# Kernel optimization log

Measured on AMD Instinct MI355X. Metric: run time of the kernel, lower is better.

Reference implementation:

```python
import jax, jax.numpy as jnp
import numpy as np

B, S, D, F, R = 128, 128, 512, 84, 32
DS = D // 8      # priori (projected) dim = 64
NE = 3           # number of RefExperts actually constructed
H = D // 64      # 8 heads for both nn.MultiheadAttention modules and feat SDPA
NEG = -1e9


def ln(x, g, b, eps=1e-5):
    m = x.mean(-1, keepdims=True)
    v = ((x - m) ** 2).mean(-1, keepdims=True)
    return (x - m) * jax.lax.rsqrt(v + eps) * g + b


def mha(q, k, v, Wi, bi, Wo, bo, h, mask=None):
    # torch nn.MultiheadAttention with packed in_proj (stored here as [D,3D])
    Dm = q.shape[-1]
    dh = Dm // h
    qp = (q @ Wi[:, :Dm] + bi[:Dm]).reshape(q.shape[0], q.shape[1], h, dh)
    kp = (k @ Wi[:, Dm:2 * Dm] + bi[Dm:2 * Dm]).reshape(k.shape[0], k.shape[1], h, dh)
    vp = (v @ Wi[:, 2 * Dm:] + bi[2 * Dm:]).reshape(v.shape[0], v.shape[1], h, dh)
    s = jnp.einsum('bqhd,bkhd->bhqk', qp, kp) / np.float32(np.sqrt(dh))
    if mask is not None:
        s = jnp.where(mask, NEG, s)
    o = jnp.einsum('bhqk,bkhd->bqhd', jax.nn.softmax(s, -1), vp)
    return o.reshape(q.shape[0], q.shape[1], Dm) @ Wo + bo


def forward(hidden_states, tag_hidden_state, feats, refs,
            W_moe, b_moe, Wg, bg, Wq_e, Wk_e, Wv_e, Wo_e,
            g_np, b_np, Wi_p, bi_p, Wo_p, bo_p, W_pe, b_pe,
            g_nh, b_nh, Wi_f, bi_f, Wo_f, bo_f,
            g_nfh, b_nfh, Wq_a, bq_a, Wk_a, bk_a, Wv_a, bv_a, Wd, bd, g_ln, b_ln):
    seq = tag_hidden_state.shape[1]
    causal = jnp.triu(jnp.ones((seq, seq), bool), 1)  # torch triu(diag=1).bool()
    # ---- MOE priori: project tags, soft-gate 3 reference cross-attn experts ----
    xs = tag_hidden_state @ W_moe + b_moe                 # [B,S,DS]
    gate = jax.nn.softmax(xs @ Wg + bg, -1)               # [B,S,NE]
    q = jnp.einsum('bsd,edk->ebsk', xs, Wq_e)             # [E,B,S,DS]
    k = jnp.einsum('ebrf,efk->ebrk', refs, Wk_e)          # [E,B,R,DS]
    v = jnp.einsum('ebrf,efk->ebrk', refs, Wv_e)
    s = jnp.einsum('ebsk,ebrk->ebsr', q, k) / np.float32(np.sqrt(DS))
    eo = jnp.einsum('ebsr,ebrk->ebsk', jax.nn.softmax(s, -1), v)
    eo = jnp.einsum('ebsk,ekm->ebsm', eo, Wo_e)           # [E,B,S,DS]
    priori = jnp.einsum('ebsd,bse->bsd', eo, gate)        # [B,S,DS]
    # ---- priori causal self-attention (pre-LN residual) ----
    npri = ln(priori, g_np, b_np)
    priori = mha(npri, npri, npri, Wi_p, bi_p, Wo_p, bo_p, H, causal) + priori
    priori = priori @ W_pe + b_pe                         # [B,S,D]
    # ---- fusion cross-attention: hidden attends to priori (causal) ----
    npri = ln(priori, g_nh, b_nh)
    hidden_states = mha(hidden_states, npri, npri, Wi_f, bi_f, Wo_f, bo_f, H, causal) + hidden_states
    # ---- feat cross-attention block (MultiHeadAttention wrapper, post-LN) ----
    nh = ln(hidden_states, g_nfh, b_nfh)
    dh = D // H
    qp = (nh @ Wq_a + bq_a).reshape(B, seq, H, dh)
    kp = (feats @ Wk_a + bk_a).reshape(B, F, H, dh)
    vp = (feats @ Wv_a + bv_a).reshape(B, F, H, dh)
    s2 = jnp.einsum('bqhd,bkhd->bhqk', qp, kp) / np.float32(np.sqrt(dh))
    ctx = jnp.einsum('bhqk,bkhd->bqhd', jax.nn.softmax(s2, -1), vp).reshape(B, seq, D)
    ctx = ctx @ Wd + bd                                   # dense; dropout is eval-mode identity
    return ln(ctx + nh, g_ln, b_ln, 1e-12)                # skip connection + post-LN (eps=1e-12)


def setup_inputs() -> dict:
    key = jax.random.key(0)
    ks = jax.random.split(key, 40)
    p = lambda i, shp: (jax.random.normal(ks[i], shp, jnp.float32) * 0.02)
    inp = {
        'hidden_states': jax.random.normal(ks[0], (B, S, D), jnp.float32),
        'tag_hidden_state': jax.random.normal(ks[1], (B, S, D), jnp.float32),
        'feats': jax.random.normal(ks[2], (B, F, D), jnp.float32),
        'refs': jax.random.normal(ks[3], (NE, B, R, D), jnp.float32),
        'W_moe': p(4, (D, DS)), 'b_moe': jnp.zeros((DS,)),
        'Wg': p(5, (DS, NE)), 'bg': jnp.zeros((NE,)),
        'Wq_e': p(6, (NE, DS, DS)), 'Wk_e': p(7, (NE, D, DS)),
        'Wv_e': p(8, (NE, D, DS)), 'Wo_e': p(9, (NE, DS, DS)),
        'g_np': jnp.ones((DS,)), 'b_np': jnp.zeros((DS,)),
        'Wi_p': p(10, (DS, 3 * DS)), 'bi_p': jnp.zeros((3 * DS,)),
        'Wo_p': p(11, (DS, DS)), 'bo_p': jnp.zeros((DS,)),
        'W_pe': p(12, (DS, D)), 'b_pe': jnp.zeros((D,)),
        'g_nh': jnp.ones((D,)), 'b_nh': jnp.zeros((D,)),
        'Wi_f': p(13, (D, 3 * D)), 'bi_f': jnp.zeros((3 * D,)),
        'Wo_f': p(14, (D, D)), 'bo_f': jnp.zeros((D,)),
        'g_nfh': jnp.ones((D,)), 'b_nfh': jnp.zeros((D,)),
        'Wq_a': p(15, (D, D)), 'bq_a': jnp.zeros((D,)),
        'Wk_a': p(16, (D, D)), 'bk_a': jnp.zeros((D,)),
        'Wv_a': p(17, (D, D)), 'bv_a': jnp.zeros((D,)),
        'Wd': p(18, (D, D)), 'bd': jnp.zeros((D,)),
        'g_ln': jnp.ones((D,)), 'b_ln': jnp.zeros((D,)),
    }
    return inp


def reference(hidden_states, tag_hidden_state, feats, refs,
              W_moe, b_moe, Wg, bg, Wq_e, Wk_e, Wv_e, Wo_e,
              g_np, b_np, Wi_p, bi_p, Wo_p, bo_p, W_pe, b_pe,
              g_nh, b_nh, Wi_f, bi_f, Wo_f, bo_f,
              g_nfh, b_nfh, Wq_a, bq_a, Wk_a, bk_a, Wv_a, bv_a, Wd, bd, g_ln, b_ln):
    return forward(hidden_states, tag_hidden_state, feats, refs,
                   W_moe, b_moe, Wg, bg, Wq_e, Wk_e, Wv_e, Wo_e,
                   g_np, b_np, Wi_p, bi_p, Wo_p, bo_p, W_pe, b_pe,
                   g_nh, b_nh, Wi_f, bi_f, Wo_f, bo_f,
                   g_nfh, b_nfh, Wq_a, bq_a, Wk_a, bk_a, Wv_a, bv_a, Wd, bd, g_ln, b_ln)
```

## Files before the change

kernel.cpp:

```cpp
#include <hip/hip_runtime.h>
#include <hip/hip_bf16.h>

typedef unsigned short u16;
typedef unsigned int   u32;
typedef __attribute__((ext_vector_type(8))) short short8;
typedef __attribute__((ext_vector_type(4))) float f32x4;

#define BBt 128
#define SS 128
#define RR 32
#define NEx 3
#define MB (1024 * 1024)

static __device__ __forceinline__ float bs2f(u16 u){ return __uint_as_float(((u32)u) << 16); }
static __device__ __forceinline__ float blo(u32 u){ return __uint_as_float(u << 16); }
static __device__ __forceinline__ float bhi(u32 u){ return __uint_as_float(u & 0xffff0000u); }
static __device__ __forceinline__ u16 f2bs(float x){
    u32 u = __float_as_uint(x);
    u += 0x7fff + ((u >> 16) & 1);
    return (u16)(u >> 16);
}
static __device__ __forceinline__ float ldany(const float* p){ return *p; }
static __device__ __forceinline__ float ldany(const u16* p){ return bs2f(*p); }

template<typename TA, typename TRes, typename TC>
__global__ __launch_bounds__(256) void gemm_mfma(
    const TA* __restrict__ A, int lda, long long sA,
    const float* __restrict__ W, int ldw, long long sW,
    const float* __restrict__ bias,
    const TRes* __restrict__ Res, int ldr,
    TC* __restrict__ C, int ldc, long long sC,
    int K, int Ncols)
{
    int bz = blockIdx.z;
    A += (long long)bz * sA;
    W += (long long)bz * sW;
    C += (long long)bz * sC;

    __shared__ __align__(16) u16 As[128][40];
    __shared__ __align__(16) u16 Bs[128][40];

    int tid = threadIdx.x;
    long long row0 = (long long)blockIdx.y * 128;
    int col0 = blockIdx.x * 128;

    int wid = tid >> 6, lane = tid & 63;
    int wm = (wid >> 1) * 64, wn = (wid & 1) * 64;
    int l15 = lane & 15, quad = lane >> 4;

    f32x4 acc[4][4];
    #pragma unroll
    for (int i = 0; i < 4; ++i)
        #pragma unroll
        for (int j = 0; j < 4; ++j)
            acc[i][j] = (f32x4){0.f, 0.f, 0.f, 0.f};

    int ar = tid >> 1, ak = (tid & 1) * 16;
    int bk0 = (tid & 15) * 2, bn0 = (tid >> 4) * 8;

    for (int kt = 0; kt < K; kt += 32) {
        {
            const TA* src = A + (row0 + ar) * lda + kt + ak;
            if constexpr (sizeof(TA) == 4) {
                u16 tmp[16];
                #pragma unroll
                for (int t = 0; t < 16; t += 4) {
                    float4 f = *(const float4*)(src + t);
                    tmp[t] = f2bs(f.x); tmp[t+1] = f2bs(f.y);
                    tmp[t+2] = f2bs(f.z); tmp[t+3] = f2bs(f.w);
                }
                *(uint4*)&As[ar][ak]     = *(const uint4*)&tmp[0];
                *(uint4*)&As[ar][ak + 8] = *(const uint4*)&tmp[8];
            } else {
                *(uint4*)&As[ar][ak]     = *(const uint4*)(src);
                *(uint4*)&As[ar][ak + 8] = *(const uint4*)(src + 8);
            }
        }
        {
            if (col0 + bn0 < Ncols) {
                const float* w0 = W + (long long)(kt + bk0) * ldw + col0 + bn0;
                const float* w1 = w0 + ldw;
                float r0[8], r1[8];
                *(float4*)&r0[0] = *(const float4*)(w0);
                *(float4*)&r0[4] = *(const float4*)(w0 + 4);
                *(float4*)&r1[0] = *(const float4*)(w1);
                *(float4*)&r1[4] = *(const float4*)(w1 + 4);
                #pragma unroll
                for (int i = 0; i < 8; ++i) {
                    u32 packed = (u32)f2bs(r0[i]) | ((u32)f2bs(r1[i]) << 16);
                    *(u32*)&Bs[bn0 + i][bk0] = packed;
                }
            } else {
                #pragma unroll
                for (int i = 0; i < 8; ++i)
                    *(u32*)&Bs[bn0 + i][bk0] = 0u;
            }
        }
        __syncthreads();

        short8 af[4], bfr[4];
        #pragma unroll
        for (int mt = 0; mt < 4; ++mt)
            af[mt] = *(const short8*)&As[wm + mt * 16 + l15][quad * 8];
        #pragma unroll
        for (int nt = 0; nt < 4; ++nt)
            bfr[nt] = *(const short8*)&Bs[wn + nt * 16 + l15][quad * 8];
        #pragma unroll
        for (int mt = 0; mt < 4; ++mt)
            #pragma unroll
            for (int nt = 0; nt < 4; ++nt)
                acc[mt][nt] = __builtin_amdgcn_mfma_f32_16x16x32_bf16(
                    af[mt], bfr[nt], acc[mt][nt], 0, 0, 0);
        __syncthreads();
    }

    #pragma unroll
    for (int mt = 0; mt < 4; ++mt) {
        #pragma unroll
        for (int r = 0; r < 4; ++r) {
            long long row = row0 + wm + mt * 16 + quad * 4 + r;
            #pragma unroll
            for (int nt = 0; nt < 4; ++nt) {
                int col = col0 + wn + nt * 16 + l15;
                if (col >= Ncols) continue;
                float v = acc[mt][nt][r];
                if (bias) v += bias[col];
                if (Res)  v += ldany(&Res[row * ldr + col]);
                if constexpr (sizeof(TC) == 4) C[row * ldc + col] = v;
                else                           C[row * ldc + col] = f2bs(v);
            }
        }
    }
}

__global__ __launch_bounds__(256) void attn_mfma_k(
    const u16* __restrict__ Q, const u16* __restrict__ K,
    const u16* __restrict__ V, u16* __restrict__ out,
    int L, int causal)
{
    int h = blockIdx.x, b = blockIdx.y;
    int tid = threadIdx.x;
    int w = tid >> 6, lane = tid & 63;
    int l15 = lane & 15, quad = lane >> 4;

    int NTP = (L + 15) >> 4;
    int Lp  = NTP * 16;
    int ntmax = causal ? (2 * w + 1) : (NTP - 1);
    int ksmax = causal ? w : (((L + 31) >> 5) - 1);

    __shared__ __align__(16) u16 vT[64][136];
    __shared__ __align__(16) u16 pool[4][32][136];
    u16 (*kS)[72] = (u16(*)[72])&pool[0][0][0];

    for (int i = tid; i < Lp * 8; i += 256) {
        int r = i >> 3, c8 = i & 7;
        uint4 val = {0u, 0u, 0u, 0u};
        if (r < L) val = *(const uint4*)&K[((long long)b * L + r) * 512 + h * 64 + c8 * 8];
        *(uint4*)&kS[r][c8 * 8] = val;
    }
    for (int i = tid; i < 512; i += 256) {
        int kp = i & 63, dg = i >> 6;
        int kv0 = kp * 2;
        if (kv0 < Lp) {
            uint4 r0 = {0u,0u,0u,0u}, r1 = {0u,0u,0u,0u};
            if (kv0 < L)     r0 = *(const uint4*)&V[((long long)b * L + kv0    ) * 512 + h * 64 + dg * 8];
            if (kv0 + 1 < L) r1 = *(const uint4*)&V[((long long)b * L + kv0 + 1) * 512 + h * 64 + dg * 8];
            u32 w0[4] = {r0.x, r0.y, r0.z, r0.w};
            u32 w1[4] = {r1.x, r1.y, r1.z, r1.w};
            #pragma unroll
            for (int j = 0; j < 4; ++j) {
                *(u32*)&vT[dg * 8 + 2 * j    ][kv0] = (w0[j] & 0xffffu) | (w1[j] << 16);
                *(u32*)&vT[dg * 8 + 2 * j + 1][kv0] = (w0[j] >> 16) | (w1[j] & 0xffff0000u);
            }
        }
    }

    short8 qf[2][2];
    #pragma unroll
    for (int mt = 0; mt < 2; ++mt)
        #pragma unroll
        for (int ks = 0; ks < 2; ++ks)
            qf[mt][ks] = *(const short8*)&Q[((long long)b * 128 + w * 32 + mt * 16 + l15) * 512
                                            + h * 64 + ks * 32 + quad * 8];
    __syncthreads();

    f32x4 sacc[2][8];
    #pragma unroll
    for (int mt = 0; mt < 2; ++mt)
        #pragma unroll
        for (int nt = 0; nt < 8; ++nt)
            sacc[mt][nt] = (f32x4){0.f, 0.f, 0.f, 0.f};
    #pragma unroll
    for (int nt = 0; nt < 8; ++nt) {
        if (nt <= ntmax) {
            short8 kf0 = *(const short8*)&kS[nt * 16 + l15][quad * 8];
            short8 kf1 = *(const short8*)&kS[nt * 16 + l15][32 + quad * 8];
            #pragma unroll
            for (int mt = 0; mt < 2; ++mt) {
                sacc[mt][nt] = __builtin_amdgcn_mfma_f32_16x16x32_bf16(qf[mt][0], kf0, sacc[mt][nt], 0, 0, 0);
                sacc[mt][nt] = __builtin_amdgcn_mfma_f32_16x16x32_bf16(qf[mt][1], kf1, sacc[mt][nt], 0, 0, 0);
            }
        }
    }

    float pm[2][4], ls[2][4];
    #pragma unroll
    for (int mt = 0; mt < 2; ++mt) {
        #pragma unroll
        for (int r = 0; r < 4; ++r) pm[mt][r] = -1e30f;
        #pragma unroll
        for (int nt = 0; nt < 8; ++nt) {
            if (nt <= ntmax) {
                int col = nt * 16 + l15;
                #pragma unroll
                for (int r = 0; r < 4; ++r) {
                    int rowq = w * 32 + mt * 16 + quad * 4 + r;
                    bool bad = (col >= L) || (causal && col > rowq);
                    float sv = bad ? -1e30f : sacc[mt][nt][r];
                    sacc[mt][nt][r] = sv;
                    pm[mt][r] = fmaxf(pm[mt][r], sv);
                }
            }
        }
        #pragma unroll
        for (int r = 0; r < 4; ++r) {
            float mx = pm[mt][r];
            #pragma unroll
            for (int o = 1; o <= 8; o <<= 1) mx = fmaxf(mx, __shfl_xor(mx, o));
            pm[mt][r] = mx * 0.125f;
            ls[mt][r] = 0.f;
        }
        #pragma unroll
        for (int nt = 0; nt < 8; ++nt) {
            if (nt <= ntmax) {
                #pragma unroll
                for (int r = 0; r < 4; ++r) {
                    float p = __expf(fmaf(sacc[mt][nt][r], 0.125f, -pm[mt][r]));
                    sacc[mt][nt][r] = p;
                    ls[mt][r] += p;
                }
            }
        }
        #pragma unroll
        for (int r = 0; r < 4; ++r) {
            float sm = ls[mt][r];
            #pragma unroll
            for (int o = 1; o <= 8; o <<= 1) sm += __shfl_xor(sm, o);
            ls[mt][r] = 1.f / sm;
        }
    }

    __syncthreads();

    u16 (*pW)[136] = (u16(*)[136])&pool[w][0][0];
    bool wl = (l15 & 1) == 0;
    #pragma unroll
    for (int mt = 0; mt < 2; ++mt)
        #pragma unroll
        for (int nt = 0; nt < 8; ++nt) {
            if (nt <= ntmax) {
                #pragma unroll
                for (int r = 0; r < 4; ++r) {
                    float pv = sacc[mt][nt][r];
                    float po = __shfl_xor(pv, 1);
                    if (wl) {
                        u32 packed = (u32)f2bs(pv) | ((u32)f2bs(po) << 16);
                        *(u32*)&pW[mt * 16 + quad * 4 + r][nt * 16 + l15] = packed;
                    }
                }
            }
        }

    f32x4 oacc[2][4];
    #pragma unroll
    for (int mt = 0; mt < 2; ++mt)
        #pragma unroll
        for (int nd = 0; nd < 4; ++nd)
            oacc[mt][nd] = (f32x4){0.f, 0.f, 0.f, 0.f};
    #pragma unroll
    for (int ks = 0; ks < 4; ++ks) {
        if (ks <= ksmax) {
            short8 pf0 = *(const short8*)&pW[l15     ][ks * 32 + quad * 8];
            short8 pf1 = *(const short8*)&pW[16 + l15][ks * 32 + quad * 8];
            #pragma unroll
            for (int nd = 0; nd < 4; ++nd) {
                short8 vf = *(const short8*)&vT[nd * 16 + l15][ks * 32 + quad * 8];
                oacc[0][nd] = __builtin_amdgcn_mfma_f32_16x16x32_bf16(pf0, vf, oacc[0][nd], 0, 0, 0);
                oacc[1][nd] = __builtin_amdgcn_mfma_f32_16x16x32_bf16(pf1, vf, oacc[1][nd], 0, 0, 0);
            }
        }
    }

    #pragma unroll
    for (int mt = 0; mt < 2; ++mt)
        #pragma unroll
        for (int nd = 0; nd < 4; ++nd)
            #pragma unroll
            for (int r = 0; r < 4; ++r) {
                float ov = oacc[mt][nd][r] * ls[mt][r];
                float oo = __shfl_xor(ov, 1);
                if (wl) {
                    long long rowq = (long long)b * 128 + w * 32 + mt * 16 + quad * 4 + r;
                    u32 packed = (u32)f2bs(ov) | ((u32)f2bs(oo) << 16);
                    *(u32*)&out[rowq * 512 + h * 64 + nd * 16 + l15] = packed;
                }
            }
}

template<typename TI, typename TO>
__global__ __launch_bounds__(256) void ln512_t(
    const TI* __restrict__ x, const float* __restrict__ g,
    const float* __restrict__ bt, TO* __restrict__ y, float eps)
{
    int row = blockIdx.x, tid = threadIdx.x;
    long long base = (long long)row * 512;
    float v0 = ldany(&x[base + tid]);
    float v1 = ldany(&x[base + 256 + tid]);
    float s = v0 + v1, ss = v0 * v0 + v1 * v1;
    #pragma unroll
    for (int o = 32; o >= 1; o >>= 1) { s += __shfl_xor(s, o); ss += __shfl_xor(ss, o); }
    __shared__ float red[2][4];
    int wave = tid >> 6, lane = tid & 63;
    if (lane == 0) { red[0][wave] = s; red[1][wave] = ss; }
    __syncthreads();
    s  = red[0][0] + red[0][1] + red[0][2] + red[0][3];
    ss = red[1][0] + red[1][1] + red[1][2] + red[1][3];
    float mean = s * (1.f / 512.f);
    float var = ss * (1.f / 512.f) - mean * mean;
    float rstd = rsqrtf(fmaxf(var, 0.f) + eps);
    float o0 = (v0 - mean) * rstd * g[tid]       + bt[tid];
    float o1 = (v1 - mean) * rstd * g[256 + tid] + bt[256 + tid];
    if constexpr (sizeof(TO) == 4) { y[base + tid] = o0; y[base + 256 + tid] = o1; }
    else { y[base + tid] = f2bs(o0); y[base + 256 + tid] = f2bs(o1); }
}

__global__ __launch_bounds__(128) void moe_attn_k(
    const float* __restrict__ qe,
    const float* __restrict__ ke,
    const float* __restrict__ ve,
    const float* __restrict__ xs,
    const float* __restrict__ Wg,
    const float* __restrict__ bg,
    float* __restrict__ geo)
{
    int e = blockIdx.x, b = blockIdx.y;
    int tid = threadIdx.x;
    __shared__ __align__(16) float kS[RR][64];
    __shared__ __align__(16) float vS[RR][64];

    {
        const float4* ks = (const float4*)&ke[((long long)e * (BBt * RR) + (long long)b * RR) * 64];
        const float4* vs = (const float4*)&ve[((long long)e * (BBt * RR) + (long long)b * RR) * 64];
        float4* kd = (float4*)&kS[0][0];
        float4* vd = (float4*)&vS[0][0];
        #pragma unroll
        for (int t = 0; t < 4; ++t) {
            kd[tid + 128 * t] = ks[tid + 128 * t];
            vd[tid + 128 * t] = vs[tid + 128 * t];
        }
    }

    long long row = (long long)b * SS + tid;
    float q[64];
    {
        const float4* qp = (const float4*)&qe[((long long)e * (BBt * SS) + row) * 64];
        #pragma unroll
        for (int t = 0; t < 16; ++t) {
            float4 f = qp[t];
            q[4*t] = f.x; q[4*t+1] = f.y; q[4*t+2] = f.z; q[4*t+3] = f.w;
        }
    }

    float l0 = bg[0], l1 = bg[1], l2 = bg[2];
    {
        const float4* xr = (const float4*)&xs[row * 64];
        #pragma unroll
        for (int t = 0; t < 16; ++t) {
            float4 f = xr[t];
            float xv[4] = {f.x, f.y, f.z, f.w};
            #pragma unroll
            for (int u = 0; u < 4; ++u) {
                int j = 4 * t + u;
                l0 = fmaf(xv[u], Wg[j * 3 + 0], l0);
                l1 = fmaf(xv[u], Wg[j * 3 + 1], l1);
                l2 = fmaf(xv[u], Wg[j * 3 + 2], l2);
            }
        }
    }
    float mg = fmaxf(l0, fmaxf(l1, l2));
    float g0 = __expf(l0 - mg), g1 = __expf(l1 - mg), g2 = __expf(l2 - mg);
    float gate = (e == 0 ? g0 : (e == 1 ? g1 : g2)) / (g0 + g1 + g2);

    __syncthreads();

    float s[RR];
    #pragma unroll
    for (int r = 0; r < RR; ++r) {
        float a0 = 0.f, a1 = 0.f, a2 = 0.f, a3 = 0.f;
        const float4* kr = (const float4*)&kS[r][0];
        #pragma unroll
        for (int t = 0; t < 16; ++t) {
            float4 f = kr[t];
            a0 = fmaf(q[4*t],   f.x, a0);
            a1 = fmaf(q[4*t+1], f.y, a1);
            a2 = fmaf(q[4*t+2], f.z, a2);
            a3 = fmaf(q[4*t+3], f.w, a3);
        }
        s[r] = ((a0 + a1) + (a2 + a3)) * 0.125f;
    }
    float m = s[0];
    #pragma unroll
    for (int r = 1; r < RR; ++r) m = fmaxf(m, s[r]);
    float l = 0.f;
    #pragma unroll
    for (int r = 0; r < RR; ++r) { s[r] = __expf(s[r] - m); l += s[r]; }
    float scale = gate / l;

    float acc[64];
    #pragma unroll
    for (int d = 0; d < 64; ++d) acc[d] = 0.f;
    #pragma unroll
    for (int r = 0; r < RR; ++r) {
        float p = s[r];
        const float4* vr = (const float4*)&vS[r][0];
        #pragma unroll
        for (int t = 0; t < 16; ++t) {
            float4 f = vr[t];
            acc[4*t]   = fmaf(p, f.x, acc[4*t]);
            acc[4*t+1] = fmaf(p, f.y, acc[4*t+1]);
            acc[4*t+2] = fmaf(p, f.z, acc[4*t+2]);
            acc[4*t+3] = fmaf(p, f.w, acc[4*t+3]);
        }
    }
    float4* op = (float4*)&geo[row * 192 + e * 64];
    #pragma unroll
    for (int t = 0; t < 16; ++t) {
        float4 f;
        f.x = acc[4*t] * scale;   f.y = acc[4*t+1] * scale;
        f.z = acc[4*t+2] * scale; f.w = acc[4*t+3] * scale;
        op[t] = f;
    }
}

__global__ __launch_bounds__(128) void attn_small_k(
    const float* __restrict__ qkv, float* __restrict__ out)
{
    int h = blockIdx.x, b = blockIdx.y;
    int tid = threadIdx.x;
    __shared__ float kS[SS][9], vS[SS][9];
    long long base = ((long long)b * SS + tid) * 192;
    #pragma unroll
    for (int d = 0; d < 8; ++d) {
        kS[tid][d] = qkv[base + 64 + h * 8 + d];
        vS[tid][d] = qkv[base + 128 + h * 8 + d];
    }
    float q[8];
    #pragma unroll
    for (int d = 0; d < 8; ++d)
        q[d] = qkv[base + h * 8 + d] * 0.35355339059327373f;
    __syncthreads();

    float m = -1e30f, l = 0.f, acc[8] = {};
    for (int j = 0; j <= tid; ++j) {
        float s = 0.f;
        #pragma unroll
        for (int d = 0; d < 8; ++d) s = fmaf(q[d], kS[j][d], s);
        float mn = fmaxf(m, s);
        float corr = __expf(m - mn);
        float p = __expf(s - mn);
        l = l * corr + p;
        #pragma unroll
        for (int d = 0; d < 8; ++d) acc[d] = fmaf(p, vS[j][d], acc[d] * corr);
        m = mn;
    }
    float inv = 1.f / l;
    #pragma unroll
    for (int d = 0; d < 8; ++d)
        out[((long long)b * SS + tid) * 64 + h * 8 + d] = acc[d] * inv;
}

__global__ __launch_bounds__(256) void ln64_k(
    const float* __restrict__ x, const float* __restrict__ g,
    const float* __restrict__ bt, float* __restrict__ y, int M)
{
    int wave = threadIdx.x >> 6, lane = threadIdx.x & 63;
    int row = blockIdx.x * 4 + wave;
    if (row >= M) return;
    long long base = (long long)row * 64;
    float v = x[base + lane];
    float s = v, ss = v * v;
    #pragma unroll
    for (int o = 32; o >= 1; o >>= 1) { s += __shfl_xor(s, o); ss += __shfl_xor(ss, o); }
    float mean = s * (1.f / 64.f);
    float var = ss * (1.f / 64.f) - mean * mean;
    float rstd = rsqrtf(fmaxf(var, 0.f) + 1e-5f);
    y[base + lane] = (v - mean) * rstd * g[lane] + bt[lane];
}

extern "C" void kernel_launch(void* const* d_in, const int* in_sizes, int n_in,
                              void* d_out, int out_size, void* d_ws, size_t ws_size,
                              hipStream_t stream)
{
    (void)in_sizes; (void)n_in; (void)out_size; (void)ws_size;
    const float* hidden = (const float*)d_in[0];
    const float* tag    = (const float*)d_in[1];
    const float* feats  = (const float*)d_in[2];
    const float* refs   = (const float*)d_in[3];
    const float* W_moe  = (const float*)d_in[4];
    const float* b_moe  = (const float*)d_in[5];
    const float* Wg     = (const float*)d_in[6];
    const float* bg     = (const float*)d_in[7];
    const float* Wq_e   = (const float*)d_in[8];
    const float* Wk_e   = (const float*)d_in[9];
    const float* Wv_e   = (const float*)d_in[10];
    const float* Wo_e   = (const float*)d_in[11];
    const float* g_np   = (const float*)d_in[12];
    const float* b_np   = (const float*)d_in[13];
    const float* Wi_p   = (const float*)d_in[14];
    const float* bi_p   = (const float*)d_in[15];
    const float* Wo_p   = (const float*)d_in[16];
    const float* bo_p   = (const float*)d_in[17];
    const float* W_pe   = (const float*)d_in[18];
    const float* b_pe   = (const float*)d_in[19];
    const float* g_nh   = (const float*)d_in[20];
    const float* b_nh   = (const float*)d_in[21];
    const float* Wi_f   = (const float*)d_in[22];
    const float* bi_f   = (const float*)d_in[23];
    const float* Wo_f   = (const float*)d_in[24];
    const float* bo_f   = (const float*)d_in[25];
    const float* g_nfh  = (const float*)d_in[26];
    const float* b_nfh  = (const float*)d_in[27];
    const float* Wq_a   = (const float*)d_in[28];
    const float* bq_a   = (const float*)d_in[29];
    const float* Wk_a   = (const float*)d_in[30];
    const float* bk_a   = (const float*)d_in[31];
    const float* Wv_a   = (const float*)d_in[32];
    const float* bv_a   = (const float*)d_in[33];
    const float* Wd     = (const float*)d_in[34];
    const float* bd     = (const float*)d_in[35];
    const float* g_ln   = (const float*)d_in[36];
    const float* b_ln   = (const float*)d_in[37];
    float* out = (float*)d_out;
    char* ob = (char*)d_out;
    char* wb = (char*)d_ws;

    u16* W0 = (u16*)(wb + 0LL * 16 * MB);
    u16* W1 = (u16*)(wb + 1LL * 16 * MB);
    u16* O0 = (u16*)(ob + 0LL * 16 * MB);
    u16* O1 = (u16*)(ob + 1LL * 16 * MB);

    float* o_xs   = (float*)(ob + 0LL  * MB);
    float* o_ke   = (float*)(ob + 4LL  * MB);
    float* o_ve   = (float*)(ob + 7LL  * MB);
    float* o_pri  = (float*)(ob + 10LL * MB);
    float* o_np64 = (float*)(ob + 14LL * MB);
    float* o_qkv  = (float*)(ob + 18LL * MB);
    float* o_attp = (float*)(ob + 0LL  * MB);
    float* o_tmp  = (float*)(ob + 4LL  * MB);
    float* o_qe   = (float*)(wb + 0LL  * MB);
    float* o_geo  = (float*)(wb + 16LL * MB);

    dim3 blk(256);
    const float* fnull = nullptr;

    gemm_mfma<float, float, float><<<dim3(1, 128), blk, 0, stream>>>(
        tag, 512, 0, W_moe, 64, 0, b_moe, fnull, 0, o_xs, 64, 0, 512, 64);
    gemm_mfma<float, float, float><<<dim3(1, 32, 3), blk, 0, stream>>>(
        refs, 512, 4096LL * 512, Wk_e, 64, 512LL * 64, nullptr, fnull, 0,
        o_ke, 64, 4096LL * 64, 512, 64);
    gemm_mfma<float, float, float><<<dim3(1, 32, 3), blk, 0, stream>>>(
        refs, 512, 4096LL * 512, Wv_e, 64, 512LL * 64, nullptr, fnull, 0,
        o_ve, 64, 4096LL * 64, 512, 64);
    gemm_mfma<float, float, float><<<dim3(1, 128, 3), blk, 0, stream>>>(
        o_xs, 64, 0, Wq_e, 64, 4096LL, nullptr, fnull, 0,
        o_qe, 64, 16384LL * 64, 64, 64);
    moe_attn_k<<<dim3(3, 128), dim3(128), 0, stream>>>(
        o_qe, o_ke, o_ve, o_xs, Wg, bg, o_geo);
    gemm_mfma<float, float, float><<<dim3(1, 128), blk, 0, stream>>>(
        o_geo, 192, 0, Wo_e, 64, 0, nullptr, fnull, 0, o_pri, 64, 0, 192, 64);

    ln64_k<<<dim3(4096), blk, 0, stream>>>(o_pri, g_np, b_np, o_np64, 16384);
    gemm_mfma<float, float, float><<<dim3(2, 128), blk, 0, stream>>>(
        o_np64, 64, 0, Wi_p, 192, 0, bi_p, fnull, 0, o_qkv, 192, 0, 64, 192);
    attn_small_k<<<dim3(8, 128), dim3(128), 0, stream>>>(o_qkv, o_attp);
    gemm_mfma<float, float, float><<<dim3(1, 128), blk, 0, stream>>>(
        o_attp, 64, 0, Wo_p, 64, 0, bo_p, o_pri, 64, o_tmp, 64, 0, 64, 64);
    gemm_mfma<float, float, u16><<<dim3(4, 128), blk, 0, stream>>>(
        o_tmp, 64, 0, W_pe, 512, 0, b_pe, fnull, 0, W0, 512, 0, 64, 512);

    ln512_t<u16, u16><<<dim3(16384), blk, 0, stream>>>(W0, g_nh, b_nh, W0, 1e-5f);
    gemm_mfma<u16, float, u16><<<dim3(4, 128), blk, 0, stream>>>(
        W0, 512, 0, Wi_f + 512, 1536, 0, bi_f + 512, fnull, 0, O1, 512, 0, 512, 512);
    gemm_mfma<u16, float, u16><<<dim3(4, 128), blk, 0, stream>>>(
        W0, 512, 0, Wi_f + 1024, 1536, 0, bi_f + 1024, fnull, 0, W1, 512, 0, 512, 512);
    gemm_mfma<float, float, u16><<<dim3(4, 128), blk, 0, stream>>>(
        hidden, 512, 0, Wi_f, 1536, 0, bi_f, fnull, 0, O0, 512, 0, 512, 512);
    attn_mfma_k<<<dim3(8, 128), dim3(256), 0, stream>>>(O0, O1, W1, W0, 128, 1);
    gemm_mfma<u16, float, u16><<<dim3(4, 128), blk, 0, stream>>>(
        W0, 512, 0, Wo_f, 512, 0, bo_f, hidden, 512, O0, 512, 0, 512, 512);

    ln512_t<u16, u16><<<dim3(16384), blk, 0, stream>>>(O0, g_nfh, b_nfh, O0, 1e-5f);
    gemm_mfma<u16, float, u16><<<dim3(4, 128), blk, 0, stream>>>(
        O0, 512, 0, Wq_a, 512, 0, bq_a, fnull, 0, O1, 512, 0, 512, 512);
    gemm_mfma<float, float, u16><<<dim3(4, 84), blk, 0, stream>>>(
        feats, 512, 0, Wk_a, 512, 0, bk_a, fnull, 0, W0, 512, 0, 512, 512);
    gemm_mfma<float, float, u16><<<dim3(4, 84), blk, 0, stream>>>(
        feats, 512, 0, Wv_a, 512, 0, bv_a, fnull, 0, W1, 512, 0, 512, 512);
    attn_mfma_k<<<dim3(8, 128), dim3(256), 0, stream>>>(O1, W0, W1, O1, 84, 0);
    gemm_mfma<u16, u16, u16><<<dim3(4, 128), blk, 0, stream>>>(
        O1, 512, 0, Wd, 512, 0, bd, O0, 512, W0, 512, 0, 512, 512);

    ln512_t<u16, float><<<dim3(16384), blk, 0, stream>>>(W0, g_ln, b_ln, out, 1e-12f);
}
```

Measured before the change: 936.7 us.

## Stream GEMM weights directly into MFMA fragments, double-buffer A, and merge sibling projections

The GEMM kernel no longer stages the fp32 weight tile through shared memory. Each wave loads its B fragments straight from global memory and packs them with the hardware v_cvt_pk_bf16 instruction. The A tile is double-buffered in LDS, with the next tile prefetched into registers during the MFMAs, so there is one barrier per k-step. Projections that share an input (K/V of the MoE refs, K/V of the Wi_f self-attn, and K/V of feats) now run as one wider launch with split outputs, cutting launches and repeated reads of the same A. In exchange, each lane issues many strided scalar weight loads, and waves sharing a column block read the same weights twice.

New measurement: 1.369 ms. 1.46x slower.

```diff
diff --git a/kernel.cpp b/kernel.cpp
--- a/kernel.cpp
+++ b/kernel.cpp
@@ -13,32 +13,34 @@
 #define MB (1024 * 1024)
 
 static __device__ __forceinline__ float bs2f(u16 u){ return __uint_as_float(((u32)u) << 16); }
-static __device__ __forceinline__ float blo(u32 u){ return __uint_as_float(u << 16); }
-static __device__ __forceinline__ float bhi(u32 u){ return __uint_as_float(u & 0xffff0000u); }
 static __device__ __forceinline__ u16 f2bs(float x){
     u32 u = __float_as_uint(x);
     u += 0x7fff + ((u >> 16) & 1);
     return (u16)(u >> 16);
 }
+static __device__ __forceinline__ u32 pkbf(float a, float b){
+    u32 r; asm("v_cvt_pk_bf16_f32 %0, %1, %2" : "=v"(r) : "v"(a), "v"(b)); return r;
+}
 static __device__ __forceinline__ float ldany(const float* p){ return *p; }
 static __device__ __forceinline__ float ldany(const u16* p){ return bs2f(*p); }
 
 template<typename TA, typename TRes, typename TC>
-__global__ __launch_bounds__(256) void gemm_mfma(
+__global__ __launch_bounds__(256) void gemm_bb(
     const TA* __restrict__ A, int lda, long long sA,
-    const float* __restrict__ W, int ldw, long long sW,
-    const float* __restrict__ bias,
+    const float* __restrict__ W, const float* __restrict__ W2, int ldw, long long sW,
+    const float* __restrict__ bias, const float* __restrict__ bias2,
     const TRes* __restrict__ Res, int ldr,
-    TC* __restrict__ C, int ldc, long long sC,
-    int K, int Ncols)
+    TC* __restrict__ C, TC* __restrict__ C2, int ldc, long long sC,
+    int K, int Ncols, int Nsplit)
 {
     int bz = blockIdx.z;
     A += (long long)bz * sA;
     W += (long long)bz * sW;
+    if (W2) W2 += (long long)bz * sW;
     C += (long long)bz * sC;
-
-    __shared__ __align__(16) u16 As[128][40];
-    __shared__ __align__(16) u16 Bs[128][40];
+    if (C2) C2 += (long long)bz * sC;
+
+    __shared__ __align__(16) u16 As[2][128][40];
 
     int tid = threadIdx.x;
     long long row0 = (long long)blockIdx.y * 128;
@@ -56,61 +58,76 @@
             acc[i][j] = (f32x4){0.f, 0.f, 0.f, 0.f};
 
     int ar = tid >> 1, ak = (tid & 1) * 16;
-    int bk0 = (tid & 15) * 2, bn0 = (tid >> 4) * 8;
-
-    for (int kt = 0; kt < K; kt += 32) {
-        {
-            const TA* src = A + (row0 + ar) * lda + kt + ak;
+
+    {
+        const TA* src = A + (row0 + ar) * lda + ak;
+        if constexpr (sizeof(TA) == 4) {
+            float4 f0 = *(const float4*)(src);
+            float4 f1 = *(const float4*)(src + 4);
+            float4 f2 = *(const float4*)(src + 8);
+            float4 f3 = *(const float4*)(src + 12);
+            u32 t0[4] = {pkbf(f0.x,f0.y), pkbf(f0.z,f0.w), pkbf(f1.x,f1.y), pkbf(f1.z,f1.w)};
+            u32 t1[4] = {pkbf(f2.x,f2.y), pkbf(f2.z,f2.w), pkbf(f3.x,f3.y), pkbf(f3.z,f3.w)};
+            *(uint4*)&As[0][ar][ak]     = *(uint4*)t0;
+            *(uint4*)&As[0][ar][ak + 8] = *(uint4*)t1;
+        } else {
+            *(uint4*)&As[0][ar][ak]     = *(const uint4*)(src);
+            *(uint4*)&As[0][ar][ak + 8] = *(const uint4*)(src + 8);
+        }
+    }
+    __syncthreads();
+
+    int nsteps = K >> 5;
+    for (int s = 0; s < nsteps; ++s) {
+        int p = s & 1;
+        uint4 st0, st1;
+        bool have = (s + 1 < nsteps);
+        if (have) {
+            const TA* src = A + (row0 + ar) * lda + ((s + 1) << 5) + ak;
             if constexpr (sizeof(TA) == 4) {
-                u16 tmp[16];
-                #pragma unroll
-                for (int t = 0; t < 16; t += 4) {
-                    float4 f = *(const float4*)(src + t);
-                    tmp[t] = f2bs(f.x); tmp[t+1] = f2bs(f.y);
-                    tmp[t+2] = f2bs(f.z); tmp[t+3] = f2bs(f.w);
+                float4 f0 = *(const float4*)(src);
+                float4 f1 = *(const float4*)(src + 4);
+                float4 f2 = *(const float4*)(src + 8);
+                float4 f3 = *(const float4*)(src + 12);
+                u32 t0[4] = {pkbf(f0.x,f0.y), pkbf(f0.z,f0.w), pkbf(f1.x,f1.y), pkbf(f1.z,f1.w)};
+                u32 t1[4] = {pkbf(f2.x,f2.y), pkbf(f2.z,f2.w), pkbf(f3.x,f3.y), pkbf(f3.z,f3.w)};
+                st0 = *(uint4*)t0; st1 = *(uint4*)t1;
+            } else {
+                st0 = *(const uint4*)(src);
+                st1 = *(const uint4*)(src + 8);
+            }
+        }
+        short8 af[4];
+        #pragma unroll
+        for (int mt = 0; mt < 4; ++mt)
+            af[mt] = *(const short8*)&As[p][wm + mt * 16 + l15][quad * 8];
+        int kb = (s << 5) + quad * 8;
+        #pragma unroll
+        for (int nt = 0; nt < 4; ++nt) {
+            int col = col0 + wn + nt * 16 + l15;
+            const float* wp = W; int wc = col;
+            if (W2 && col >= Nsplit) { wp = W2; wc = col - Nsplit; }
+            bool ok = (col < Ncols);
+            const float* pw = wp + (long long)kb * ldw + wc;
+            union { u32 u[4]; short8 s8; } bb;
+            #pragma unroll
+            for (int i = 0; i < 4; ++i) {
+                float w0 = 0.f, w1 = 0.f;
+                if (ok) {
+                    w0 = pw[(2 * i) * ldw];
+                    w1 = pw[(2 * i + 1) * ldw];
                 }
-                *(uint4*)&As[ar][ak]     = *(const uint4*)&tmp[0];
-                *(uint4*)&As[ar][ak + 8] = *(const uint4*)&tmp[8];
-            } else {
-                *(uint4*)&As[ar][ak]     = *(const uint4*)(src);
-                *(uint4*)&As[ar][ak + 8] = *(const uint4*)(src + 8);
-            }
-        }
-        {
-            if (col0 + bn0 < Ncols) {
-                const float* w0 = W + (long long)(kt + bk0) * ldw + col0 + bn0;
-                const float* w1 = w0 + ldw;
-                float r0[8], r1[8];
-                *(float4*)&r0[0] = *(const float4*)(w0);
-                *(float4*)&r0[4] = *(const float4*)(w0 + 4);
-                *(float4*)&r1[0] = *(const float4*)(w1);
-                *(float4*)&r1[4] = *(const float4*)(w1 + 4);
-                #pragma unroll
-                for (int i = 0; i < 8; ++i) {
-                    u32 packed = (u32)f2bs(r0[i]) | ((u32)f2bs(r1[i]) << 16);
-                    *(u32*)&Bs[bn0 + i][bk0] = packed;
-                }
-            } else {
-                #pragma unroll
-                for (int i = 0; i < 8; ++i)
-                    *(u32*)&Bs[bn0 + i][bk0] = 0u;
-            }
-        }
-        __syncthreads();
-
-        short8 af[4], bfr[4];
-        #pragma unroll
-        for (int mt = 0; mt < 4; ++mt)
-            af[mt] = *(const short8*)&As[wm + mt * 16 + l15][quad * 8];
-        #pragma unroll
-        for (int nt = 0; nt < 4; ++nt)
-            bfr[nt] = *(const short8*)&Bs[wn + nt * 16 + l15][quad * 8];
-        #pragma unroll
-        for (int mt = 0; mt < 4; ++mt)
-            #pragma unroll
-            for (int nt = 0; nt < 4; ++nt)
+                bb.u[i] = pkbf(w0, w1);
+            }
+            #pragma unroll
+            for (int mt = 0; mt < 4; ++mt)
                 acc[mt][nt] = __builtin_amdgcn_mfma_f32_16x16x32_bf16(
-                    af[mt], bfr[nt], acc[mt][nt], 0, 0, 0);
+                    af[mt], bb.s8, acc[mt][nt], 0, 0, 0);
+        }
+        if (have) {
+            *(uint4*)&As[p ^ 1][ar][ak]     = st0;
+            *(uint4*)&As[p ^ 1][ar][ak + 8] = st1;
+        }
         __syncthreads();
     }
 
@@ -124,10 +141,13 @@
                 int col = col0 + wn + nt * 16 + l15;
                 if (col >= Ncols) continue;
                 float v = acc[mt][nt][r];
-                if (bias) v += bias[col];
-                if (Res)  v += ldany(&Res[row * ldr + col]);
-                if constexpr (sizeof(TC) == 4) C[row * ldc + col] = v;
-                else                           C[row * ldc + col] = f2bs(v);
+                if (bias2 && col >= Nsplit) v += bias2[col - Nsplit];
+                else if (bias)              v += bias[col];
+                if (Res) v += ldany(&Res[row * ldr + col]);
+                TC* dst = (C2 && col >= Nsplit) ? (C2 + row * ldc + (col - Nsplit))
+                                                : (C  + row * ldc + col);
+                if constexpr (sizeof(TC) == 4) *dst = v;
+                else                           *dst = f2bs(v);
             }
         }
     }
@@ -562,53 +582,59 @@
 
     dim3 blk(256);
     const float* fnull = nullptr;
-
-    gemm_mfma<float, float, float><<<dim3(1, 128), blk, 0, stream>>>(
-        tag, 512, 0, W_moe, 64, 0, b_moe, fnull, 0, o_xs, 64, 0, 512, 64);
-    gemm_mfma<float, float, float><<<dim3(1, 32, 3), blk, 0, stream>>>(
-        refs, 512, 4096LL * 512, Wk_e, 64, 512LL * 64, nullptr, fnull, 0,
-        o_ke, 64, 4096LL * 64, 512, 64);
-    gemm_mfma<float, float, float><<<dim3(1, 32, 3), blk, 0, stream>>>(
-        refs, 512, 4096LL * 512, Wv_e, 64, 512LL * 64, nullptr, fnull, 0,
-        o_ve, 64, 4096LL * 64, 512, 64);
-    gemm_mfma<float, float, float><<<dim3(1, 128, 3), blk, 0, stream>>>(
-        o_xs, 64, 0, Wq_e, 64, 4096LL, nullptr, fnull, 0,
-        o_qe, 64, 16384LL * 64, 64, 64);
+    float* f32null = nullptr;
+    u16* u16null = nullptr;
+
+    gemm_bb<float, float, float><<<dim3(1, 128), blk, 0, stream>>>(
+        tag, 512, 0, W_moe, fnull, 64, 0, b_moe, fnull, fnull, 0,
+        o_xs, f32null, 64, 0, 512, 64, 0);
+    gemm_bb<float, float, float><<<dim3(1, 32, 3), blk, 0, stream>>>(
+        refs, 512, 4096LL * 512, Wk_e, Wv_e, 64, 512LL * 64, fnull, fnull, fnull, 0,
+        o_ke, o_ve, 64, 4096LL * 64, 512, 128, 64);
+    gemm_bb<float, float, float><<<dim3(1, 128, 3), blk, 0, stream>>>(
+        o_xs, 64, 0, Wq_e, fnull, 64, 4096LL, fnull, fnull, fnull, 0,
+        o_qe, f32null, 64, 16384LL * 64, 64, 64, 0);
     moe_attn_k<<<dim3(3, 128), dim3(128), 0, stream>>>(
         o_qe, o_ke, o_ve, o_xs, Wg, bg, o_geo);
-    gemm_mfma<float, float, float><<<dim3(1, 128), blk, 0, stream>>>(
-        o_geo, 192, 0, Wo_e, 64, 0, nullptr, fnull, 0, o_pri, 64, 0, 192, 64);
+    gemm_bb<float, float, float><<<dim3(1, 128), blk, 0, stream>>>(
+        o_geo, 192, 0, Wo_e, fnull, 64, 0, fnull, fnull, fnull, 0,
+        o_pri, f32null, 64, 0, 192, 64, 0);
 
     ln64_k<<<dim3(4096), blk, 0, stream>>>(o_pri, g_np, b_np, o_np64, 16384);
-    gemm_mfma<float, float, float><<<dim3(2, 128), blk, 0, stream>>>(
-        o_np64, 64, 0, Wi_p, 192, 0, bi_p, fnull, 0, o_qkv, 192, 0, 64, 192);
+    gemm_bb<float, float, float><<<dim3(2, 128), blk, 0, stream>>>(
+        o_np64, 64, 0, Wi_p, fnull, 192, 0, bi_p, fnull, fnull, 0,
+        o_qkv, f32null, 192, 0, 64, 192, 0);
     attn_small_k<<<dim3(8, 128), dim3(128), 0, stream>>>(o_qkv, o_attp);
-    gemm_mfma<float, float, float><<<dim3(1, 128), blk, 0, stream>>>(
-        o_attp, 64, 0, Wo_p, 64, 0, bo_p, o_pri, 64, o_tmp, 64, 0, 64, 64);
-    gemm_mfma<float, float, u16><<<dim3(4, 128), blk, 0, stream>>>(
-        o_tmp, 64, 0, W_pe, 512, 0, b_pe, fnull, 0, W0, 512, 0, 64, 512);
+    gemm_bb<float, float, float><<<dim3(1, 128), blk, 0, stream>>>(
+        o_attp, 64, 0, Wo_p, fnull, 64, 0, bo_p, fnull, o_pri, 64,
+        o_tmp, f32null, 64, 0, 64, 64, 0);
+    gemm_bb<float, float, u16><<<dim3(4, 128), blk, 0, stream>>>(
+        o_tmp, 64, 0, W_pe, fnull, 512, 0, b_pe, fnull, fnull, 0,
+        W0, u16null, 512, 0, 64, 512, 0);
 
     ln512_t<u16, u16><<<dim3(16384), blk, 0, stream>>>(W0, g_nh, b_nh, W0, 1e-5f);
-    gemm_mfma<u16, float, u16><<<dim3(4, 128), blk, 0, stream>>>(
-        W0, 512, 0, Wi_f + 512, 1536, 0, bi_f + 512, fnull, 0, O1, 512, 0, 512, 512);
-    gemm_mfma<u16, float, u16><<<dim3(4, 128), blk, 0, stream>>>(
-        W0, 512, 0, Wi_f + 1024, 1536, 0, bi_f + 1024, fnull, 0, W1, 512, 0, 512, 512);
-    gemm_mfma<float, float, u16><<<dim3(4, 128), blk, 0, stream>>>(
-        hidden, 512, 0, Wi_f, 1536, 0, bi_f, fnull, 0, O0, 512, 0, 512, 512);
+    gemm_bb<u16, float, u16><<<dim3(8, 128), blk, 0, stream>>>(
+        W0, 512, 0, Wi_f + 512, fnull, 1536, 0, bi_f + 512, fnull, fnull, 0,
+        O1, W1, 512, 0, 512, 1024, 512);
+    gemm_bb<float, float, u16><<<dim3(4, 128), blk, 0, stream>>>(
+        hidden, 512, 0, Wi_f, fnull, 1536, 0, bi_f, fnull, fnull, 0,
+        O0, u16null, 512, 0, 512, 512, 0);
     attn_mfma_k<<<dim3(8, 128), dim3(256), 0, stream>>>(O0, O1, W1, W0, 128, 1);
-    gemm_mfma<u16, float, u16><<<dim3(4, 128), blk, 0, stream>>>(
-        W0, 512, 0, Wo_f, 512, 0, bo_f, hidden, 512, O0, 512, 0, 512, 512);
+    gemm_bb<u16, float, u16><<<dim3(4, 128), blk, 0, stream>>>(
+        W0, 512, 0, Wo_f, fnull, 512, 0, bo_f, fnull, hidden, 512,
+        O0, u16null, 512, 0, 512, 512, 0);
 
     ln512_t<u16, u16><<<dim3(16384), blk, 0, stream>>>(O0, g_nfh, b_nfh, O0, 1e-5f);
-    gemm_mfma<u16, float, u16><<<dim3(4, 128), blk, 0, stream>>>(
-        O0, 512, 0, Wq_a, 512, 0, bq_a, fnull, 0, O1, 512, 0, 512, 512);
-    gemm_mfma<float, float, u16><<<dim3(4, 84), blk, 0, stream>>>(
-        feats, 512, 0, Wk_a, 512, 0, bk_a, fnull, 0, W0, 512, 0, 512, 512);
-    gemm_mfma<float, float, u16><<<dim3(4, 84), blk, 0, stream>>>(
-        feats, 512, 0, Wv_a, 512, 0, bv_a, fnull, 0, W1, 512, 0, 512, 512);
+    gemm_bb<u16, float, u16><<<dim3(4, 128), blk, 0, stream>>>(
+        O0, 512, 0, Wq_a, fnull, 512, 0, bq_a, fnull, fnull, 0,
+        O1, u16null, 512, 0, 512, 512, 0);
+    gemm_bb<float, float, u16><<<dim3(8, 84), blk, 0, stream>>>(
+        feats, 512, 0, Wk_a, Wv_a, 512, 0, bk_a, bv_a, fnull, 0,
+        W0, W1, 512, 0, 512, 1024, 512);
     attn_mfma_k<<<dim3(8, 128), dim3(256), 0, stream>>>(O1, W0, W1, O1, 84, 0);
-    gemm_mfma<u16, u16, u16><<<dim3(4, 128), blk, 0, stream>>>(
-        O1, 512, 0, Wd, 512, 0, bd, O0, 512, W0, 512, 0, 512, 512);
+    gemm_bb<u16, u16, u16><<<dim3(4, 128), blk, 0, stream>>>(
+        O1, 512, 0, Wd, fnull, 512, 0, bd, fnull, O0, 512,
+        W0, u16null, 512, 0, 512, 512, 0);
 
     ln512_t<u16, float><<<dim3(16384), blk, 0, stream>>>(W0, g_ln, b_ln, out, 1e-12f);
 }
```

## Pre-transpose weights to bf16 and use vectorized GEMM loads with fused K/V projection

Applied to the files above, without the earlier changes.

Adds a small transpose-and-convert kernel that writes each weight matrix as bf16 in N-major layout. A new GEMM variant can then load B tiles with 16-byte vector reads, and it converts fp32 A with packed bf16 conversion instructions. The expert K and V projections are merged into one launch that splits its output columns into two buffers. The cost is extra transpose launches on every call, plus workspace buffers reused across stages, which adds aliasing risk.

Result: faster. 887.5 us (-5.3%).

```diff
diff --git a/kernel.cpp b/kernel.cpp
--- a/kernel.cpp
+++ b/kernel.cpp
@@ -13,15 +13,37 @@
 #define MB (1024 * 1024)
 
 static __device__ __forceinline__ float bs2f(u16 u){ return __uint_as_float(((u32)u) << 16); }
-static __device__ __forceinline__ float blo(u32 u){ return __uint_as_float(u << 16); }
-static __device__ __forceinline__ float bhi(u32 u){ return __uint_as_float(u & 0xffff0000u); }
 static __device__ __forceinline__ u16 f2bs(float x){
     u32 u = __float_as_uint(x);
     u += 0x7fff + ((u >> 16) & 1);
     return (u16)(u >> 16);
 }
+static __device__ __forceinline__ u32 pkbf(float a, float b){
+    u32 r; asm("v_cvt_pk_bf16_f32 %0, %1, %2" : "=v"(r) : "v"(a), "v"(b)); return r;
+}
 static __device__ __forceinline__ float ldany(const float* p){ return *p; }
 static __device__ __forceinline__ float ldany(const u16* p){ return bs2f(*p); }
+
+__global__ __launch_bounds__(256) void tr_bf(
+    const float* __restrict__ src, int lds_, long long sSrc,
+    u16* __restrict__ dst, long long sDst, int ldd)
+{
+    int z = blockIdx.z;
+    src += (long long)z * sSrc;
+    dst += (long long)z * sDst;
+    int n0 = blockIdx.x * 32, k0 = blockIdx.y * 32;
+    __shared__ u16 t[32][33];
+    int c = threadIdx.x & 31, r0 = threadIdx.x >> 5;
+    #pragma unroll
+    for (int i = 0; i < 4; ++i) {
+        int r = r0 + i * 8;
+        t[r][c] = f2bs(src[(long long)(k0 + r) * lds_ + n0 + c]);
+    }
+    __syncthreads();
+    int rr = threadIdx.x >> 3, kk = (threadIdx.x & 7) * 4;
+    u16 o[4] = { t[kk][rr], t[kk+1][rr], t[kk+2][rr], t[kk+3][rr] };
+    *(uint2*)&dst[(long long)(n0 + rr) * ldd + k0 + kk] = *(uint2*)o;
+}
 
 template<typename TA, typename TRes, typename TC>
 __global__ __launch_bounds__(256) void gemm_mfma(
@@ -128,6 +150,110 @@
                 if (Res)  v += ldany(&Res[row * ldr + col]);
                 if constexpr (sizeof(TC) == 4) C[row * ldc + col] = v;
                 else                           C[row * ldc + col] = f2bs(v);
+            }
+        }
+    }
+}
+
+template<typename TA, typename TRes, typename TC>
+__global__ __launch_bounds__(256) void gemm_v5(
+    const TA* __restrict__ A, int lda, long long sA,
+    const u16* __restrict__ WT, long long sW,
+    const float* __restrict__ bias, const float* __restrict__ bias2,
+    const TRes* __restrict__ Res, int ldr,
+    TC* __restrict__ C, TC* __restrict__ C2, int ldc, long long sC,
+    int K, int Ncols, int Nsplit)
+{
+    int bz = blockIdx.z;
+    A += (long long)bz * sA;
+    WT += (long long)bz * sW;
+    C += (long long)bz * sC;
+    if (C2) C2 += (long long)bz * sC;
+
+    __shared__ __align__(16) u16 As[128][40];
+    __shared__ __align__(16) u16 Bs[128][40];
+
+    int tid = threadIdx.x;
+    long long row0 = (long long)blockIdx.y * 128;
+    int col0 = blockIdx.x * 128;
+
+    int wid = tid >> 6, lane = tid & 63;
+    int wm = (wid >> 1) * 64, wn = (wid & 1) * 64;
+    int l15 = lane & 15, quad = lane >> 4;
+
+    f32x4 acc[4][4];
+    #pragma unroll
+    for (int i = 0; i < 4; ++i)
+        #pragma unroll
+        for (int j = 0; j < 4; ++j)
+            acc[i][j] = (f32x4){0.f, 0.f, 0.f, 0.f};
+
+    int ar = tid >> 1, ak = (tid & 1) * 16;
+
+    for (int kt = 0; kt < K; kt += 32) {
+        {
+            const TA* src = A + (row0 + ar) * lda + kt + ak;
+            if constexpr (sizeof(TA) == 4) {
+                float4 f0 = *(const float4*)(src);
+                float4 f1 = *(const float4*)(src + 4);
+                float4 f2 = *(const float4*)(src + 8);
+                float4 f3 = *(const float4*)(src + 12);
+                u32 t[8] = {pkbf(f0.x,f0.y), pkbf(f0.z,f0.w), pkbf(f1.x,f1.y), pkbf(f1.z,f1.w),
+                            pkbf(f2.x,f2.y), pkbf(f2.z,f2.w), pkbf(f3.x,f3.y), pkbf(f3.z,f3.w)};
+                *(uint4*)&As[ar][ak]     = *(uint4*)&t[0];
+                *(uint4*)&As[ar][ak + 8] = *(uint4*)&t[4];
+            } else {
+                *(uint4*)&As[ar][ak]     = *(const uint4*)(src);
+                *(uint4*)&As[ar][ak + 8] = *(const uint4*)(src + 8);
+            }
+        }
+        {
+            int nr = col0 + ar;
+            if (nr < Ncols) {
+                const u16* ws = WT + (long long)nr * K + kt + ak;
+                *(uint4*)&Bs[ar][ak]     = *(const uint4*)(ws);
+                *(uint4*)&Bs[ar][ak + 8] = *(const uint4*)(ws + 8);
+            } else {
+                uint4 z = {0u, 0u, 0u, 0u};
+                *(uint4*)&Bs[ar][ak] = z;
+                *(uint4*)&Bs[ar][ak + 8] = z;
+            }
+        }
+        __syncthreads();
+
+        short8 af[4], bfr[4];
+        #pragma unroll
+        for (int mt = 0; mt < 4; ++mt)
+            af[mt] = *(const short8*)&As[wm + mt * 16 + l15][quad * 8];
+        #pragma unroll
+        for (int nt = 0; nt < 4; ++nt)
+            bfr[nt] = *(const short8*)&Bs[wn + nt * 16 + l15][quad * 8];
+        #pragma unroll
+        for (int mt = 0; mt < 4; ++mt)
+            #pragma unroll
+            for (int nt = 0; nt < 4; ++nt)
+                acc[mt][nt] = __builtin_amdgcn_mfma_f32_16x16x32_bf16(
+                    af[mt], bfr[nt], acc[mt][nt], 0, 0, 0);
+        __syncthreads();
+    }
+
+    #pragma unroll
+    for (int mt = 0; mt < 4; ++mt) {
+        #pragma unroll
+        for (int r = 0; r < 4; ++r) {
+            long long row = row0 + wm + mt * 16 + quad * 4 + r;
+            #pragma unroll
+            for (int nt = 0; nt < 4; ++nt) {
+                int col = col0 + wn + nt * 16 + l15;
+                if (col >= Ncols) continue;
+                float v = acc[mt][nt][r];
+                if (bias2 && col >= Nsplit) v += bias2[col - Nsplit];
+                else if (bias)              v += bias[col];
+                if (Res) v += ldany(&Res[row * ldr + col]);
+                TC* dst = (C2 && col >= Nsplit) ? (C2 + row * ldc + (col - Nsplit))
+                                                : (C  + row * ldc + col);
+                if constexpr (sizeof(TC) == 4) *dst = v;
+                else                           *dst = f2bs(v);
             }
         }
     }
@@ -560,17 +686,29 @@
     float* o_qe   = (float*)(wb + 0LL  * MB);
     float* o_geo  = (float*)(wb + 16LL * MB);
 
+    u16* WT_moe = (u16*)(wb + 30LL * MB);
+    u16* WT_kve = (u16*)(wb + 30LL * MB + 131072);
+    u16* WT_ikv = (u16*)(ob + 0LL  * MB);
+    u16* WT_iq  = (u16*)(wb + 0LL  * MB);
+    u16* WT_of  = (u16*)(ob + 16LL * MB);
+    u16* WT_qa  = (u16*)(wb + 16LL * MB);
+    u16* WT_d   = (u16*)(wb + 16LL * MB);
+
     dim3 blk(256);
     const float* fnull = nullptr;
-
-    gemm_mfma<float, float, float><<<dim3(1, 128), blk, 0, stream>>>(
-        tag, 512, 0, W_moe, 64, 0, b_moe, fnull, 0, o_xs, 64, 0, 512, 64);
-    gemm_mfma<float, float, float><<<dim3(1, 32, 3), blk, 0, stream>>>(
-        refs, 512, 4096LL * 512, Wk_e, 64, 512LL * 64, nullptr, fnull, 0,
-        o_ke, 64, 4096LL * 64, 512, 64);
-    gemm_mfma<float, float, float><<<dim3(1, 32, 3), blk, 0, stream>>>(
-        refs, 512, 4096LL * 512, Wv_e, 64, 512LL * 64, nullptr, fnull, 0,
-        o_ve, 64, 4096LL * 64, 512, 64);
+    float* f32null = nullptr;
+    u16* u16null = nullptr;
+
+    tr_bf<<<dim3(2, 16), blk, 0, stream>>>(W_moe, 64, 0, WT_moe, 0, 512);
+    tr_bf<<<dim3(2, 16, 3), blk, 0, stream>>>(Wk_e, 64, 512LL * 64, WT_kve, 128LL * 512, 512);
+    tr_bf<<<dim3(2, 16, 3), blk, 0, stream>>>(Wv_e, 64, 512LL * 64, WT_kve + 64 * 512, 128LL * 512, 512);
+
+    gemm_v5<float, float, float><<<dim3(1, 128), blk, 0, stream>>>(
+        tag, 512, 0, WT_moe, 0, b_moe, fnull, fnull, 0,
+        o_xs, f32null, 64, 0, 512, 64, 0);
+    gemm_v5<float, float, float><<<dim3(1, 32, 3), blk, 0, stream>>>(
+        refs, 512, 4096LL * 512, WT_kve, 128LL * 512, fnull, fnull, fnull, 0,
+        o_ke, o_ve, 64, 4096LL * 64, 512, 128, 64);
     gemm_mfma<float, float, float><<<dim3(1, 128, 3), blk, 0, stream>>>(
         o_xs, 64, 0, Wq_e, 64, 4096LL, nullptr, fnull, 0,
         o_qe, 64, 16384LL * 64, 64, 64);
@@ -589,26 +727,37 @@
         o_tmp, 64, 0, W_pe, 512, 0, b_pe, fnull, 0, W0, 512, 0, 64, 512);
 
     ln512_t<u16, u16><<<dim3(16384), blk, 0, stream>>>(W0, g_nh, b_nh, W0, 1e-5f);
-    gemm_mfma<u16, float, u16><<<dim3(4, 128), blk, 0, stream>>>(
-        W0, 512, 0, Wi_f + 512, 1536, 0, bi_f + 512, fnull, 0, O1, 512, 0, 512, 512);
-    gemm_mfma<u16, float, u16><<<dim3(4, 128), blk, 0, stream>>>(
-        W0, 512, 0, Wi_f + 1024, 1536, 0, bi_f + 1024, fnull, 0, W1, 512, 0, 512, 512);
-    gemm_mfma<float, float, u16><<<dim3(4, 128), blk, 0, stream>>>(
-        hidden, 512, 0, Wi_f, 1536, 0, bi_f, fnull, 0, O0, 512, 0, 512, 512);
+    tr_bf<<<dim3(32, 16), blk, 0, stream>>>(Wi_f + 512, 1536, 0, WT_ikv, 0, 512);
+    gemm_v5<u16, float, u16><<<dim3(4, 128), blk, 0, stream>>>(
+        W0, 512, 0, WT_ikv, 0, bi_f + 512, fnull, fnull, 0,
+        O1, u16null, 512, 0, 512, 512, 0);
+    gemm_v5<u16, float, u16><<<dim3(4, 128), blk, 0, stream>>>(
+        W0, 512, 0, WT_ikv + 512 * 512, 0, bi_f + 1024, fnull, fnull, 0,
+        W1, u16null, 512, 0, 512, 512, 0);
+    tr_bf<<<dim3(16, 16), blk, 0, stream>>>(Wi_f, 1536, 0, WT_iq, 0, 512);
+    gemm_v5<float, float, u16><<<dim3(4, 128), blk, 0, stream>>>(
+        hidden, 512, 0, WT_iq, 0, bi_f, fnull, fnull, 0,
+        O0, u16null, 512, 0, 512, 512, 0);
     attn_mfma_k<<<dim3(8, 128), dim3(256), 0, stream>>>(O0, O1, W1, W0, 128, 1);
-    gemm_mfma<u16, float, u16><<<dim3(4, 128), blk, 0, stream>>>(
-        W0, 512, 0, Wo_f, 512, 0, bo_f, hidden, 512, O0, 512, 0, 512, 512);
+    tr_bf<<<dim3(16, 16), blk, 0, stream>>>(Wo_f, 512, 0, WT_of, 0, 512);
+    gemm_v5<u16, float, u16><<<dim3(4, 128), blk, 0, stream>>>(
+        W0, 512, 0, WT_of, 0, bo_f, fnull, hidden, 512,
+        O0, u16null, 512, 0, 512, 512, 0);
 
     ln512_t<u16, u16><<<dim3(16384), blk, 0, stream>>>(O0, g_nfh, b_nfh, O0, 1e-5f);
-    gemm_mfma<u16, float, u16><<<dim3(4, 128), blk, 0, stream>>>(
-        O0, 512, 0, Wq_a, 512, 0, bq_a, fnull, 0, O1, 512, 0, 512, 512);
+    tr_bf<<<dim3(16, 16), blk, 0, stream>>>(Wq_a, 512, 0, WT_qa, 0, 512);
+    gemm_v5<u16, float, u16><<<dim3(4, 128), blk, 0, stream>>>(
+        O0, 512, 0, WT_qa, 0, bq_a, fnull, fnull, 0,
+        O1, u16null, 512, 0, 512, 512, 0);
     gemm_mfma<float, float, u16><<<dim3(4, 84), blk, 0, stream>>>(
         feats, 512, 0, Wk_a, 512, 0, bk_a, fnull, 0, W0, 512, 0, 512, 512);
     gemm_mfma<float, float, u16><<<dim3(4, 84), blk, 0, stream>>>(
         feats, 512, 0, Wv_a, 512, 0, bv_a, fnull, 0, W1, 512, 0, 512, 512);
     attn_mfma_k<<<dim3(8, 128), dim3(256), 0, stream>>>(O1, W0, W1, O1, 84, 0);
-    gemm_mfma<u16, u16, u16><<<dim3(4, 128), blk, 0, stream>>>(
-        O1, 512, 0, Wd, 512, 0, bd, O0, 512, W0, 512, 0, 512, 512);
+    tr_bf<<<dim3(16, 16), blk, 0, stream>>>(Wd, 512, 0, WT_d, 0, 512);
+    gemm_v5<u16, u16, u16><<<dim3(4, 128), blk, 0, stream>>>(
+        O1, 512, 0, WT_d, 0, bd, fnull, O0, 512,
+        W0, u16null, 512, 0, 512, 512, 0);
 
     ln512_t<u16, float><<<dim3(16384), blk, 0, stream>>>(W0, g_ln, b_ln, out, 1e-12f);
 }
```
